# Kernel tuning notes

Hardware: AMD Instinct MI355X
Metric: run time of the kernel (lower is better)

Reference implementation:

```python
import jax, jax.numpy as jnp
import numpy as np
import math

N = 12288
IN_MAIN, IN_MOD = 64, 128
NC_INNER, NC_QK, OUT_MAIN = 16, 8, 64

def setup_inputs() -> dict:
    key = jax.random.key(0)
    ks = jax.random.split(key, 8)
    s = lambda fan_in: 1.0 / np.sqrt(fan_in)
    return {
        "x_main": jax.random.normal(ks[0], (N, IN_MAIN), dtype=jnp.float32),
        "x_mod": jax.random.normal(ks[1], (N, IN_MOD), dtype=jnp.float32),
        "xyz": jax.random.uniform(ks[2], (N, 3), dtype=jnp.float32),
        # MLP E: [in_main+in_mod -> nc_inner -> nc_inner], bias=False (weights stored [in, out])
        "W_e1": jax.random.uniform(ks[3], (IN_MAIN + IN_MOD, NC_INNER), jnp.float32, -s(IN_MAIN + IN_MOD), s(IN_MAIN + IN_MOD)),
        "W_e2": jax.random.uniform(ks[4], (NC_INNER, NC_INNER), jnp.float32, -s(NC_INNER), s(NC_INNER)),
        "W_q": jax.random.uniform(ks[5], (NC_INNER, NC_QK), jnp.float32, -s(NC_INNER), s(NC_INNER)),
        "W_k": jax.random.uniform(ks[6], (NC_INNER, NC_QK), jnp.float32, -s(NC_INNER), s(NC_INNER)),
        "W_v": jax.random.uniform(ks[7], (NC_INNER, OUT_MAIN), jnp.float32, -s(NC_INNER), s(NC_INNER)),
    }

def reference(x_main, x_mod, xyz, W_e1, W_e2, W_q, W_k, W_v):
    # concat 3D + 2D features: [N, in_main+in_mod]
    x = jnp.concatenate((x_main, x_mod), axis=-1)
    # MLP E (bias-free Linear + ReLU per layer): [N, nc_inner]
    h = jax.nn.relu(jax.nn.relu(x @ W_e1) @ W_e2)
    Q = h @ W_q  # [N, nc_qk]
    K = h @ W_k  # [N, nc_qk]
    V = h @ W_v  # [N, out_main]
    scale = 1.0 / math.sqrt(NC_QK)
    scores = (Q @ K.T) * scale          # [N, N] full global attention
    attn = jax.nn.softmax(scores, axis=1)
    return attn @ V                     # [N, out_main]
```

## Files before the change

kernel.cpp:

```cpp
#include <hip/hip_runtime.h>
#include <stdint.h>


#define NN 12288

typedef float    f32x16 __attribute__((ext_vector_type(16)));
typedef short    s16x8  __attribute__((ext_vector_type(8)));
typedef unsigned short u16;

#define MFMA_32x32x16_BF16 __builtin_amdgcn_mfma_f32_32x32x16_bf16

#define OFF_QB   0u
#define OFF_VT   196608u
#define OFF_PO   2162688u

__device__ __forceinline__ float bf2f(u16 s) {
    union { unsigned int u; float f; } c; c.u = ((unsigned int)s) << 16; return c.f;
}
__device__ __forceinline__ u16 f2bf(float f) {
    union { float f; unsigned int u; } c; c.f = f;
    return (u16)((c.u + 0x8000u) >> 16);
}
__device__ __forceinline__ unsigned int pk2(float a, float b) {
    union { float f; unsigned int u; } ca, cb; ca.f = a; cb.f = b;
    return ((ca.u + 0x8000u) >> 16) | ((cb.u + 0x8000u) & 0xffff0000u);
}
__device__ __forceinline__ unsigned int pkbf(float a, float b) {
#if __has_builtin(__builtin_amdgcn_cvt_pk_bf16_f32)
    auto r = __builtin_amdgcn_cvt_pk_bf16_f32(a, b);
    union { decltype(r) v; unsigned int u; } c; c.v = r; return c.u;
#else
    return pk2(a, b);
#endif
}
__device__ __forceinline__ f32x16 zf16() {
    f32x16 z;
#pragma unroll
    for (int i = 0; i < 16; ++i) z[i] = 0.f;
    return z;
}
__device__ __forceinline__ s16x8 zs8() {
    s16x8 z;
#pragma unroll
    for (int i = 0; i < 8; ++i) z[i] = 0;
    return z;
}

union U8 { s16x8 v; unsigned int u[4]; };
union QV { uint4 q; s16x8 v; };

__global__ __launch_bounds__(256) void k1_qkv(
    const void* __restrict__ xmain, const void* __restrict__ xmod,
    const void* __restrict__ we1, const void* __restrict__ we2,
    const void* __restrict__ wqp, const void* __restrict__ wkp,
    const void* __restrict__ wvp,
    u16* __restrict__ qb, u16* __restrict__ vt)
{
    __shared__ float wf[4608];
    __shared__ int   sflag;
    __shared__ float lh1[64][4][17];
    __shared__ float lh2[64][17];

    const int t = threadIdx.x;
    const int r = t >> 2;
    const int p = t & 3;
    const int row = blockIdx.x * 64 + r;

    if (t == 0) sflag = 0;
    __syncthreads();
    {
        float v = bf2f(((const u16*)xmod)[2 * t]);
        if (fabsf(v) > 16.f) atomicAdd(&sflag, 1);
    }
    __syncthreads();
    const int isf32 = (sflag > 8);

    const float SCL = 0.51006979f;
    if (isf32) {
        const float* a1 = (const float*)we1; const float* a2 = (const float*)we2;
        const float* aq = (const float*)wqp; const float* ak = (const float*)wkp;
        const float* av = (const float*)wvp;
        for (int i = t; i < 4608; i += 256) {
            if      (i < 3072) wf[i] = a1[i];
            else if (i < 3328) wf[i] = a2[i - 3072];
            else if (i < 3456) wf[i] = aq[i - 3328] * SCL;
            else if (i < 3584) wf[i] = ak[i - 3456];
            else               wf[i] = av[i - 3584];
        }
    } else {
        const u16* a1 = (const u16*)we1; const u16* a2 = (const u16*)we2;
        const u16* aq = (const u16*)wqp; const u16* ak = (const u16*)wkp;
        const u16* av = (const u16*)wvp;
        for (int i = t; i < 4608; i += 256) {
            if      (i < 3072) wf[i] = bf2f(a1[i]);
            else if (i < 3328) wf[i] = bf2f(a2[i - 3072]);
            else if (i < 3456) wf[i] = bf2f(aq[i - 3328]) * SCL;
            else if (i < 3584) wf[i] = bf2f(ak[i - 3456]);
            else               wf[i] = bf2f(av[i - 3584]);
        }
    }
    __syncthreads();

    const float* __restrict__ W1 = wf;
    const float* __restrict__ W2 = wf + 3072;
    const float* __restrict__ Wq = wf + 3328;
    const float* __restrict__ Wk = wf + 3456;
    const float* __restrict__ Wv = wf + 3584;

    float h1p[16];
#pragma unroll
    for (int o = 0; o < 16; ++o) h1p[o] = 0.f;

    if (isf32) {
#pragma unroll
        for (int cc = 0; cc < 12; ++cc) {
            const int c = p + cc * 4;
            float4 xv = (c < 16)
                ? ((const float4*)xmain)[(size_t)row * 16 + c]
                : ((const float4*)xmod)[(size_t)row * 32 + (c - 16)];
            float xs[4] = {xv.x, xv.y, xv.z, xv.w};
#pragma unroll
            for (int j = 0; j < 4; ++j) {
                const float* wr = W1 + (c * 4 + j) * 16;
#pragma unroll
                for (int o = 0; o < 16; ++o) h1p[o] += xs[j] * wr[o];
            }
        }
    } else {
#pragma unroll
        for (int cc = 0; cc < 12; ++cc) {
            const int c = p + cc * 4;
            uint2 xv = (c < 16)
                ? ((const uint2*)xmain)[(size_t)row * 16 + c]
                : ((const uint2*)xmod)[(size_t)row * 32 + (c - 16)];
            float xs[4] = { bf2f((u16)(xv.x & 0xffff)), bf2f((u16)(xv.x >> 16)),
                            bf2f((u16)(xv.y & 0xffff)), bf2f((u16)(xv.y >> 16)) };
#pragma unroll
            for (int j = 0; j < 4; ++j) {
                const float* wr = W1 + (c * 4 + j) * 16;
#pragma unroll
                for (int o = 0; o < 16; ++o) h1p[o] += xs[j] * wr[o];
            }
        }
    }
#pragma unroll
    for (int o = 0; o < 16; ++o) lh1[r][p][o] = h1p[o];
    __syncthreads();

    float h1[16];
#pragma unroll
    for (int o = 0; o < 16; ++o)
        h1[o] = fmaxf(lh1[r][0][o] + lh1[r][1][o] + lh1[r][2][o] + lh1[r][3][o], 0.f);

#pragma unroll
    for (int oo = 0; oo < 4; ++oo) {
        const int o = p * 4 + oo;
        float s = 0.f;
#pragma unroll
        for (int j = 0; j < 16; ++j) s += h1[j] * W2[j * 16 + o];
        lh2[r][o] = fmaxf(s, 0.f);
    }
    __syncthreads();

    float h2[16];
#pragma unroll
    for (int j = 0; j < 16; ++j) h2[j] = lh2[r][j];

    {
        float q0 = 0.f, q1 = 0.f, k0 = 0.f, k1 = 0.f;
        const int o = 2 * p;
#pragma unroll
        for (int j = 0; j < 16; ++j) {
            q0 += h2[j] * Wq[j * 8 + o];
            q1 += h2[j] * Wq[j * 8 + o + 1];
            k0 += h2[j] * Wk[j * 8 + o];
            k1 += h2[j] * Wk[j * 8 + o + 1];
        }
        ((unsigned int*)qb)[(size_t)row * 4 + p] = pk2(q0, q1);
        ((unsigned int*)vt)[(size_t)(row >> 6) * 2304 + 2048 +
                            (row & 63) * 4 + p] = pk2(k0, k1);
    }

    {
        const int ch = row >> 6, tI = (row >> 5) & 1, kk = row & 31;
        const int b   = kk >> 4, kk4 = kk & 15;
        const int hh  = (kk4 >> 2) & 1;
        const int jj  = (kk4 & 3) + 4 * (kk4 >> 3);
        const size_t cbase = (size_t)ch * 4608 + (size_t)(tI * 4 + b) * 512
                           + hh * 256 + jj;
#pragma unroll
        for (int c16 = 0; c16 < 16; ++c16) {
            const int c = p * 16 + c16;
            float v = 0.f;
#pragma unroll
            for (int j = 0; j < 16; ++j) v += h2[j] * Wv[j * 64 + c];
            vt[cbase + (size_t)(c >> 5) * 1024 + (c & 31) * 8] = f2bf(v);
        }
    }
}


__global__ __launch_bounds__(256, 3) void k2_attn(
    const u16* __restrict__ qb, const u16* __restrict__ vt,
    u16* __restrict__ po, float* __restrict__ pl,
    int nsplit, int ntile)
{
    __shared__ float sf[4][2178];

    const int tid  = threadIdx.x;
    const int lane = tid & 63;
    const int half = lane >> 5;
    const int l31  = lane & 31;
    const int w    = tid >> 6;
    const int qB   = (blockIdx.x % 96) * 128;
    const int sp   = blockIdx.x / 96;
    const int myq  = qB + 32 * w;
    const int key_start = sp * (NN / nsplit);
    const char* vbase = (const char*)vt + (size_t)(key_start >> 6) * 9216;

    const f32x16 Z = zf16();
    s16x8 qf = zs8();
    if (!half) qf = *(const s16x8*)(qb + (size_t)(myq + l31) * 8);

    s16x8 ones;
#pragma unroll
    for (int i = 0; i < 8; ++i) ones[i] = (short)0x3F80;

    f32x16 acc0 = Z, acc1 = Z, accl = Z;

    QV kaA, f00A, f10A, f01A, f11A;
    QV kaB, f00B, f10B, f01B, f11B;

#define LDT(gt, ka, f00, f10, f01, f11) do {                                  \
    const char* cb_ = vbase + (size_t)((gt) >> 1) * 9216 + ((gt) & 1) * 4096; \
    (f00).q = *(const uint4*)(cb_ +        lane * 16);                        \
    (f01).q = *(const uint4*)(cb_ + 1024 + lane * 16);                        \
    (f10).q = *(const uint4*)(cb_ + 2048 + lane * 16);                        \
    (f11).q = *(const uint4*)(cb_ + 3072 + lane * 16);                        \
    (ka).q  = *(const uint4*)(vbase + (size_t)((gt) >> 1) * 9216 + 8192       \
                              + ((gt) & 1) * 512 + l31 * 16);                 \
} while (0)

#define TILE(ka, f00, f10, f01, f11) do {                                     \
    f32x16 S_ = MFMA_32x32x16_BF16((ka).v, qf, Z, 0, 0, 0);                   \
    float pr_[8];                                                             \
    U8 p0_, p1_;                                                              \
    _Pragma("unroll")                                                         \
    for (int r_ = 0; r_ < 8; ++r_) pr_[r_] = __builtin_amdgcn_exp2f(S_[r_]);  \
    _Pragma("unroll")                                                         \
    for (int i_ = 0; i_ < 4; ++i_)                                            \
        p0_.u[i_] = pkbf(pr_[2 * i_], pr_[2 * i_ + 1]);                       \
    __builtin_amdgcn_s_setprio(1);                                            \
    accl = MFMA_32x32x16_BF16(ones, p0_.v, accl, 0, 0, 0);                    \
    acc0 = MFMA_32x32x16_BF16((f00).v, p0_.v, acc0, 0, 0, 0);                 \
    acc1 = MFMA_32x32x16_BF16((f10).v, p0_.v, acc1, 0, 0, 0);                 \
    __builtin_amdgcn_s_setprio(0);                                            \
    _Pragma("unroll")                                                         \
    for (int r_ = 0; r_ < 8; ++r_) pr_[r_] = __builtin_amdgcn_exp2f(S_[r_ + 8]);\
    _Pragma("unroll")                                                         \
    for (int i_ = 0; i_ < 4; ++i_)                                            \
        p1_.u[i_] = pkbf(pr_[2 * i_], pr_[2 * i_ + 1]);                       \
    __builtin_amdgcn_s_setprio(1);                                            \
    accl = MFMA_32x32x16_BF16(ones, p1_.v, accl, 0, 0, 0);                    \
    acc0 = MFMA_32x32x16_BF16((f01).v, p1_.v, acc0, 0, 0, 0);                 \
    acc1 = MFMA_32x32x16_BF16((f11).v, p1_.v, acc1, 0, 0, 0);                 \
    __builtin_amdgcn_s_setprio(0);                                            \
} while (0)

    LDT(0, kaA, f00A, f10A, f01A, f11A);
    int gt = 0;
    for (; gt + 2 < ntile; gt += 2) {
        LDT(gt + 1, kaB, f00B, f10B, f01B, f11B);
        TILE(kaA, f00A, f10A, f01A, f11A);
        LDT(gt + 2, kaA, f00A, f10A, f01A, f11A);
        TILE(kaB, f00B, f10B, f01B, f11B);
    }
    LDT(gt + 1, kaB, f00B, f10B, f01B, f11B);
    TILE(kaA, f00A, f10A, f01A, f11A);
    TILE(kaB, f00B, f10B, f01B, f11B);

#undef LDT
#undef TILE

    const float ls = accl[0];

    float* sfw = &sf[w][0];
#pragma unroll
    for (int r = 0; r < 16; ++r) {
        const int c = (r & 3) + 8 * (r >> 2) + 4 * half;
        sfw[c * 33 + l31]        = acc0[r];
        sfw[(32 + c) * 33 + l31] = acc1[r];
    }
    if (lane < 32) sfw[2112 + l31] = ls;

    u16* poS = po + (size_t)sp * (NN * 64);
    const int lq  = lane >> 1;
    const int cb0 = (lane & 1) * 32;
    unsigned int u[16];
#pragma unroll
    for (int i = 0; i < 16; ++i)
        u[i] = pkbf(sfw[(cb0 + 2 * i) * 33 + lq],
                    sfw[(cb0 + 2 * i + 1) * 33 + lq]);
    u16* dst = poS + (size_t)(myq + lq) * 64 + cb0;
    *(uint4*)(dst)      = make_uint4(u[0],  u[1],  u[2],  u[3]);
    *(uint4*)(dst + 8)  = make_uint4(u[4],  u[5],  u[6],  u[7]);
    *(uint4*)(dst + 16) = make_uint4(u[8],  u[9],  u[10], u[11]);
    *(uint4*)(dst + 24) = make_uint4(u[12], u[13], u[14], u[15]);
    if (lane < 32)
        pl[(size_t)sp * NN + myq + l31] = sfw[2112 + l31];
}

__global__ __launch_bounds__(256) void k3_norm(
    const u16* __restrict__ po, const float* __restrict__ pl,
    float4* __restrict__ out, int nsplit)
{
    const int i = blockIdx.x * 256 + threadIdx.x;
    const int row = i >> 4;
    const int c0 = (i & 15) * 4;
    float l = 0.f;
    float o0 = 0.f, o1 = 0.f, o2 = 0.f, o3 = 0.f;
    for (int s = 0; s < nsplit; ++s) {
        l += pl[(size_t)s * NN + row];
        uint2 p = *(const uint2*)(po + (size_t)s * (NN * 64) +
                                  (size_t)row * 64 + c0);
        o0 += bf2f((u16)(p.x & 0xffff)); o1 += bf2f((u16)(p.x >> 16));
        o2 += bf2f((u16)(p.y & 0xffff)); o3 += bf2f((u16)(p.y >> 16));
    }
    const float rl = 1.0f / l;
    out[i] = make_float4(o0 * rl, o1 * rl, o2 * rl, o3 * rl);
}

extern "C" void kernel_launch(void* const* d_in, const int* in_sizes, int n_in,
                              void* d_out, int out_size, void* d_ws, size_t ws_size,
                              hipStream_t stream)
{
    const void* xmain = d_in[0];
    const void* xmod  = d_in[1];
    const void* we1   = d_in[3];
    const void* we2   = d_in[4];
    const void* wq    = d_in[5];
    const void* wk    = d_in[6];
    const void* wv    = d_in[7];

    char* ws = (char*)d_ws;
    u16*   qb   = (u16*)  (ws + OFF_QB);
    u16*   vt   = (u16*)  (ws + OFF_VT);

    int S = 8;
    while (S > 1) {
        size_t need = (size_t)OFF_PO + (size_t)S * (NN * 64 * 2) +
                      (size_t)S * (NN * 4);
        if (ws_size >= need) break;
        S >>= 1;
    }
    u16*   po = (u16*)(ws + OFF_PO);
    float* pl = (float*)(ws + OFF_PO + (size_t)S * (NN * 64 * 2));
    const int ntile = NN / (32 * S);

    k1_qkv<<<192, 256, 0, stream>>>(xmain, xmod, we1, we2, wq, wk, wv,
                                    qb, vt);
    k2_attn<<<96 * S, 256, 0, stream>>>(qb, vt, po, pl, S, ntile);
    k3_norm<<<768, 256, 0, stream>>>(po, pl, (float4*)d_out, S);
}
```

Before: 126.7 us.

## Compute softmax row sums on VALU and deepen tile prefetch to three buffers

Drops the 'ones' MFMA that accumulated the softmax denominator. The exp values are now summed in registers with scalar adds, followed by a cross-half shuffle reduction. The load pipeline also moves from double to triple buffering, keeping two tiles in flight ahead of compute. This trades a third of the MFMA work per tile for extra VALU adds and more registers, which may lower occupancy. The triple-buffer tail also assumes the tile count fits the 3-step loop (ntile ≡ 0 mod 3 or similar); otherwise tiles could be skipped or overrun.

```diff
diff --git a/kernel.cpp b/kernel.cpp
--- a/kernel.cpp
+++ b/kernel.cpp
@@ -222,14 +222,12 @@
     s16x8 qf = zs8();
     if (!half) qf = *(const s16x8*)(qb + (size_t)(myq + l31) * 8);
 
-    s16x8 ones;
-#pragma unroll
-    for (int i = 0; i < 8; ++i) ones[i] = (short)0x3F80;
-
-    f32x16 acc0 = Z, acc1 = Z, accl = Z;
+    f32x16 acc0 = Z, acc1 = Z;
+    float ls0 = 0.f, ls1 = 0.f;
 
     QV kaA, f00A, f10A, f01A, f11A;
     QV kaB, f00B, f10B, f01B, f11B;
+    QV kaC, f00C, f10C, f01C, f11C;
 
 #define LDT(gt, ka, f00, f10, f01, f11) do {                                  \
     const char* cb_ = vbase + (size_t)((gt) >> 1) * 9216 + ((gt) & 1) * 4096; \
@@ -246,43 +244,53 @@
     float pr_[8];                                                             \
     U8 p0_, p1_;                                                              \
     _Pragma("unroll")                                                         \
-    for (int r_ = 0; r_ < 8; ++r_) pr_[r_] = __builtin_amdgcn_exp2f(S_[r_]);  \
+    for (int r_ = 0; r_ < 8; ++r_) {                                          \
+        pr_[r_] = __builtin_amdgcn_exp2f(S_[r_]);                             \
+        ls0 += pr_[r_];                                                       \
+    }                                                                         \
     _Pragma("unroll")                                                         \
     for (int i_ = 0; i_ < 4; ++i_)                                            \
         p0_.u[i_] = pkbf(pr_[2 * i_], pr_[2 * i_ + 1]);                       \
     __builtin_amdgcn_s_setprio(1);                                            \
-    accl = MFMA_32x32x16_BF16(ones, p0_.v, accl, 0, 0, 0);                    \
     acc0 = MFMA_32x32x16_BF16((f00).v, p0_.v, acc0, 0, 0, 0);                 \
     acc1 = MFMA_32x32x16_BF16((f10).v, p0_.v, acc1, 0, 0, 0);                 \
     __builtin_amdgcn_s_setprio(0);                                            \
     _Pragma("unroll")                                                         \
-    for (int r_ = 0; r_ < 8; ++r_) pr_[r_] = __builtin_amdgcn_exp2f(S_[r_ + 8]);\
+    for (int r_ = 0; r_ < 8; ++r_) {                                          \
+        pr_[r_] = __builtin_amdgcn_exp2f(S_[r_ + 8]);                         \
+        ls1 += pr_[r_];                                                       \
+    }                                                                         \
     _Pragma("unroll")                                                         \
     for (int i_ = 0; i_ < 4; ++i_)                                            \
         p1_.u[i_] = pkbf(pr_[2 * i_], pr_[2 * i_ + 1]);                       \
     __builtin_amdgcn_s_setprio(1);                                            \
-    accl = MFMA_32x32x16_BF16(ones, p1_.v, accl, 0, 0, 0);                    \
     acc0 = MFMA_32x32x16_BF16((f01).v, p1_.v, acc0, 0, 0, 0);                 \
     acc1 = MFMA_32x32x16_BF16((f11).v, p1_.v, acc1, 0, 0, 0);                 \
     __builtin_amdgcn_s_setprio(0);                                            \
 } while (0)
 
     LDT(0, kaA, f00A, f10A, f01A, f11A);
+    LDT(1, kaB, f00B, f10B, f01B, f11B);
+
     int gt = 0;
-    for (; gt + 2 < ntile; gt += 2) {
-        LDT(gt + 1, kaB, f00B, f10B, f01B, f11B);
+    for (; gt + 5 <= ntile; gt += 3) {
+        LDT(gt + 2, kaC, f00C, f10C, f01C, f11C);
         TILE(kaA, f00A, f10A, f01A, f11A);
-        LDT(gt + 2, kaA, f00A, f10A, f01A, f11A);
+        LDT(gt + 3, kaA, f00A, f10A, f01A, f11A);
         TILE(kaB, f00B, f10B, f01B, f11B);
-    }
-    LDT(gt + 1, kaB, f00B, f10B, f01B, f11B);
+        LDT(gt + 4, kaB, f00B, f10B, f01B, f11B);
+        TILE(kaC, f00C, f10C, f01C, f11C);
+    }
+    LDT(gt + 2, kaC, f00C, f10C, f01C, f11C);
     TILE(kaA, f00A, f10A, f01A, f11A);
     TILE(kaB, f00B, f10B, f01B, f11B);
+    TILE(kaC, f00C, f10C, f01C, f11C);
 
 #undef LDT
 #undef TILE
 
-    const float ls = accl[0];
+    float ls = ls0 + ls1;
+    ls += __shfl_xor(ls, 32, 64);
 
     float* sfw = &sf[w][0];
 #pragma unroll
```

Measured after the change: 127.1 us. No clear change (+0.3%).
